# Kernel optimization log

Measured on AMD Instinct MI355X. Metric: run time of the kernel, lower is better.

## Reference

```python
import jax, jax.numpy as jnp
import numpy as np

B, F, S, H1, H2 = 4096, 512, 32, 64, 32


def setup_inputs() -> dict:
    key = jax.random.key(0)
    ks = jax.random.split(key, 9)
    x = jax.random.normal(ks[0], (B, F), dtype=jnp.float32)
    # ExU layer init: truncated_normal(mean=4, std=0.5) on weight, std=0.5 on bias
    W0 = 4.0 + 0.5 * jax.random.normal(ks[1], (F, S, S), dtype=jnp.float32)
    b0 = 0.5 * jax.random.normal(ks[2], (F, S), dtype=jnp.float32)
    # ReLU hidden layers: xavier-ish weights, small biases
    W1 = jax.random.normal(ks[3], (F, S, H1), dtype=jnp.float32) * np.sqrt(2.0 / (S + H1))
    b1 = 0.5 * jax.random.normal(ks[4], (F, S), dtype=jnp.float32)
    W2 = jax.random.normal(ks[5], (F, H1, H2), dtype=jnp.float32) * np.sqrt(2.0 / (H1 + H2))
    b2 = 0.5 * jax.random.normal(ks[6], (F, H1), dtype=jnp.float32)
    Wl = jax.random.normal(ks[7], (F, H2), dtype=jnp.float32) * np.sqrt(2.0 / (H2 + 1))
    out_bias = jnp.zeros((1,), dtype=jnp.float32)
    return {"x": x, "W0": W0, "b0": b0, "W1": W1, "b1": b1,
            "W2": W2, "b2": b2, "Wl": Wl, "out_bias": out_bias}


def reference(x, W0, b0, W1, b1, W2, b2, Wl, out_bias):
    # ExU shallow layer per feature: clip((x_f - b0_f) @ exp(W0_f), 0, 1)
    # x[:, :, None] - b0 broadcasts scalar feature to (B, F, S)
    h = jnp.clip(jnp.einsum('bfs,fsh->bfh', x[:, :, None] - b0[None], jnp.exp(W0)), 0.0, 1.0)
    # ReLU hidden layers: relu((h - b) @ W)
    h = jax.nn.relu(jnp.einsum('bfs,fsh->bfh', h - b1[None], W1))   # (B, F, H1)
    h = jax.nn.relu(jnp.einsum('bfh,fho->bfo', h - b2[None], W2))   # (B, F, H2)
    # per-feature Linear(H2 -> 1, no bias), concatenated over features
    f_out = jnp.einsum('bfo,fo->bf', h, Wl)                          # (B, F)
    # forward_type == 'sum' (feature_dropout is identity at inference)
    return f_out.sum(axis=-1) + out_bias[0], f_out
```

## Files before the change

kernel.cpp:

```cpp
#include <hip/hip_runtime.h>

typedef __attribute__((ext_vector_type(8))) short short8;
typedef __attribute__((ext_vector_type(4))) float f32x4;
typedef unsigned int uint32;

namespace {
constexpr int F = 512, NB = 4096;
constexpr int RB = 1024;
constexpr int FPB = 4;
constexpr int NFQ = F / FPB;
constexpr size_t OFF_W1F  = 0;
constexpr size_t OFF_W2F  = OFF_W1F + (size_t)F * 4 * 64 * 16;
constexpr size_t OFF_TAB  = OFF_W2F + (size_t)F * 4 * 64 * 16;
constexpr size_t OFF_PART = OFF_TAB + (size_t)F * 160 * 4;
constexpr size_t WS_NEED  = OFF_PART + (size_t)NFQ * NB * 4;
}

__device__ __forceinline__ uint32 cvtpk(float lo, float hi) {
    uint32 r;
    asm("v_cvt_pk_bf16_f32 %0, %1, %2" : "=v"(r) : "v"(lo), "v"(hi));
    return r;
}
__device__ __forceinline__ float clip01(float v) {
    return __builtin_amdgcn_fmed3f(v, 0.f, 1.f);
}

__global__ __launch_bounds__(256) void nam_prep(
    const float* __restrict__ W0, const float* __restrict__ b0,
    const float* __restrict__ W1, const float* __restrict__ b1,
    const float* __restrict__ W2, const float* __restrict__ b2,
    char* __restrict__ ws)
{
    const int f = blockIdx.x;
    const int t = threadIdx.x;
    const int lane = t & 63, w = t >> 6, g = lane >> 4, rr = lane & 15;

    __shared__ float LW[2048];
    __shared__ float red[256], red2[256];

    const float* W0f = W0 + (size_t)f * 1024;
    const float* W1f = W1 + (size_t)f * 2048;
    const float* W2f = W2 + (size_t)f * 2048;
    float* tab = (float*)(ws + OFF_TAB) + (size_t)f * 160;
    union U8 { uint32 u[4]; short8 s8; };

    *(float4*)&LW[t * 4] = *(const float4*)&W0f[t * 4];
    __syncthreads();
    {
        int j = t & 31, sc = t >> 5;
        float a = 0.f, c = 0.f;
#pragma unroll
        for (int k = 0; k < 4; ++k) {
            int s = sc * 4 + k;
            float e = expf(LW[s * 32 + j]);
            a += e; c += b0[f * 32 + s] * e;
        }
        red[sc * 32 + j] = a; red2[sc * 32 + j] = c;
    }
    __syncthreads();
    if (t < 32) {
        float a = 0.f, c = 0.f;
#pragma unroll
        for (int k = 0; k < 8; ++k) { a += red[k * 32 + t]; c += red2[k * 32 + t]; }
        tab[t] = a; tab[32 + t] = -c;
    }
    __syncthreads();

    *(float4*)&LW[t * 4]        = *(const float4*)&W1f[t * 4];
    *(float4*)&LW[1024 + t * 4] = *(const float4*)&W1f[1024 + t * 4];
    __syncthreads();
    {
        int j = t & 63, sc = t >> 6;
        float d = 0.f;
#pragma unroll
        for (int k = 0; k < 8; ++k) {
            int s = sc * 8 + k;
            d += b1[f * 32 + s] * LW[s * 64 + j];
        }
        red[sc * 64 + j] = d;
    }
    {
        int mi = w;
        int col = 32 * (mi & 1) + 8 * (rr >> 2) + 4 * (mi >> 1) + (rr & 3);
        int base = (8 * g) * 64 + col;
        U8 v;
        v.u[0] = cvtpk(LW[base],       LW[base + 64]);
        v.u[1] = cvtpk(LW[base + 128], LW[base + 192]);
        v.u[2] = cvtpk(LW[base + 256], LW[base + 320]);
        v.u[3] = cvtpk(LW[base + 384], LW[base + 448]);
        ((short8*)(ws + OFF_W1F))[((size_t)f * 4 + mi) * 64 + lane] = v.s8;
    }
    __syncthreads();
    if (t < 64) {
        float d = red[t] + red[64 + t] + red[128 + t] + red[192 + t];
        int dst = 32 * ((t >> 2) & 1) + 16 * (t >> 5) + 4 * ((t >> 3) & 3) + (t & 3);
        tab[64 + dst] = -d;
    }
    __syncthreads();

    *(float4*)&LW[t * 4]        = *(const float4*)&W2f[t * 4];
    *(float4*)&LW[1024 + t * 4] = *(const float4*)&W2f[1024 + t * 4];
    __syncthreads();
    {
        int o = t & 31, hc = t >> 5;
        float d = 0.f;
#pragma unroll
        for (int k = 0; k < 8; ++k) {
            int h = hc * 8 + k;
            d += b2[f * 64 + h] * LW[h * 32 + o];
        }
        red[hc * 32 + o] = d;
    }
    {
        int m2 = w >> 1, kc = w & 1;
        int base = (32 * kc + 8 * g) * 32 + 16 * m2 + rr;
        U8 v;
        v.u[0] = cvtpk(LW[base],       LW[base + 32]);
        v.u[1] = cvtpk(LW[base + 64],  LW[base + 96]);
        v.u[2] = cvtpk(LW[base + 128], LW[base + 160]);
        v.u[3] = cvtpk(LW[base + 192], LW[base + 224]);
        ((short8*)(ws + OFF_W2F))[((size_t)f * 4 + m2 * 2 + kc) * 64 + lane] = v.s8;
    }
    __syncthreads();
    if (t < 32) {
        float d = 0.f;
#pragma unroll
        for (int k = 0; k < 8; ++k) d += red[k * 32 + t];
        tab[128 + t] = -d;
    }
}

__device__ __forceinline__ void tile_compute(
    float xv, const short8* w1f, const short8 (&w2f)[2][2],
    const f32x4& A0, const f32x4& A1, const f32x4& C0, const f32x4& C1,
    const f32x4* nd1, const f32x4* nd2, f32x4& c0, f32x4& c1)
{
    union U8 { uint32 u[4]; short8 s8; };
    U8 hb;
    hb.u[0] = cvtpk(clip01(fmaf(xv, A0[0], C0[0])), clip01(fmaf(xv, A0[1], C0[1])));
    hb.u[1] = cvtpk(clip01(fmaf(xv, A0[2], C0[2])), clip01(fmaf(xv, A0[3], C0[3])));
    hb.u[2] = cvtpk(clip01(fmaf(xv, A1[0], C1[0])), clip01(fmaf(xv, A1[1], C1[1])));
    hb.u[3] = cvtpk(clip01(fmaf(xv, A1[2], C1[2])), clip01(fmaf(xv, A1[3], C1[3])));
    short8 b0f = hb.s8;

    f32x4 a0 = __builtin_amdgcn_mfma_f32_16x16x32_bf16(w1f[0], b0f, nd1[0], 0, 0, 0);
    f32x4 a1 = __builtin_amdgcn_mfma_f32_16x16x32_bf16(w1f[1], b0f, nd1[1], 0, 0, 0);
    f32x4 a2 = __builtin_amdgcn_mfma_f32_16x16x32_bf16(w1f[2], b0f, nd1[2], 0, 0, 0);
    f32x4 a3 = __builtin_amdgcn_mfma_f32_16x16x32_bf16(w1f[3], b0f, nd1[3], 0, 0, 0);

    U8 r0, r1;
    r0.u[0] = cvtpk(fmaxf(a0[0], 0.f), fmaxf(a0[1], 0.f));
    r0.u[1] = cvtpk(fmaxf(a0[2], 0.f), fmaxf(a0[3], 0.f));
    r0.u[2] = cvtpk(fmaxf(a2[0], 0.f), fmaxf(a2[1], 0.f));
    r0.u[3] = cvtpk(fmaxf(a2[2], 0.f), fmaxf(a2[3], 0.f));
    r1.u[0] = cvtpk(fmaxf(a1[0], 0.f), fmaxf(a1[1], 0.f));
    r1.u[1] = cvtpk(fmaxf(a1[2], 0.f), fmaxf(a1[3], 0.f));
    r1.u[2] = cvtpk(fmaxf(a3[0], 0.f), fmaxf(a3[1], 0.f));
    r1.u[3] = cvtpk(fmaxf(a3[2], 0.f), fmaxf(a3[3], 0.f));

    c0 = __builtin_amdgcn_mfma_f32_16x16x32_bf16(w2f[0][0], r0.s8, nd2[0], 0, 0, 0);
    c0 = __builtin_amdgcn_mfma_f32_16x16x32_bf16(w2f[0][1], r1.s8, c0, 0, 0, 0);
    c1 = __builtin_amdgcn_mfma_f32_16x16x32_bf16(w2f[1][0], r0.s8, nd2[1], 0, 0, 0);
    c1 = __builtin_amdgcn_mfma_f32_16x16x32_bf16(w2f[1][1], r1.s8, c1, 0, 0, 0);
}

__global__ __launch_bounds__(256, 2) void nam_main(
    const float* __restrict__ x, const float* __restrict__ Wl,
    const char* __restrict__ ws, float* __restrict__ fout, float* __restrict__ part)
{
    const int fq = blockIdx.y;
    const int f0 = fq * FPB;
    const int rbase = blockIdx.x * RB;
    const int t = threadIdx.x;
    const int w = t >> 6, lane = t & 63;
    const int g = lane >> 4, rr = lane & 15;
    const int f = f0 + w;

    __shared__ float sx[FPB * RB];
    __shared__ float sfo[FPB * RB];

#pragma unroll
    for (int kk = 0; kk < 4; ++kk) {
        int r = t + 256 * kk;
        float4 v = *(const float4*)(x + (size_t)(rbase + r) * F + f0);
        sx[0 * RB + r] = v.x; sx[1 * RB + r] = v.y;
        sx[2 * RB + r] = v.z; sx[3 * RB + r] = v.w;
    }

    const short8* w1img = (const short8*)(ws + OFF_W1F);
    const short8* w2img = (const short8*)(ws + OFF_W2F);
    short8 w1f[4], w2f[2][2];
#pragma unroll
    for (int mi = 0; mi < 4; ++mi) w1f[mi] = w1img[((size_t)f * 4 + mi) * 64 + lane];
#pragma unroll
    for (int m2 = 0; m2 < 2; ++m2)
#pragma unroll
        for (int kc = 0; kc < 2; ++kc)
            w2f[m2][kc] = w2img[((size_t)f * 4 + m2 * 2 + kc) * 64 + lane];

    const f32x4* tabv = (const f32x4*)((const float*)(ws + OFF_TAB) + (size_t)f * 160);
    f32x4 A0 = tabv[2 * g], A1 = tabv[2 * g + 1];
    f32x4 C0 = tabv[8 + 2 * g], C1 = tabv[8 + 2 * g + 1];
    f32x4 nd1[4];
#pragma unroll
    for (int mi = 0; mi < 4; ++mi) nd1[mi] = tabv[16 + 4 * mi + g];
    f32x4 nd2[2];
#pragma unroll
    for (int m2 = 0; m2 < 2; ++m2) nd2[m2] = tabv[32 + 4 * m2 + g];
    f32x4 wl0 = *(const f32x4*)(Wl + f * 32 + 4 * g);
    f32x4 wl1 = *(const f32x4*)(Wl + f * 32 + 16 + 4 * g);

    __syncthreads();

    const float* sxf = sx + w * RB;
    float* sfof = sfo + w * RB;

    for (int k = 0; k < 32; ++k) {
        float xv0 = sxf[32 * k + rr];
        float xv1 = sxf[32 * k + 16 + rr];
        f32x4 c00, c01, c10, c11;
        tile_compute(xv0, w1f, w2f, A0, A1, C0, C1, nd1, nd2, c00, c01);
        tile_compute(xv1, w1f, w2f, A0, A1, C0, C1, nd1, nd2, c10, c11);

        float p0 = 0.f, p1 = 0.f;
#pragma unroll
        for (int r = 0; r < 4; ++r) {
            p0 = fmaf(fmaxf(c00[r], 0.f), wl0[r], p0);
            p0 = fmaf(fmaxf(c01[r], 0.f), wl1[r], p0);
            p1 = fmaf(fmaxf(c10[r], 0.f), wl0[r], p1);
            p1 = fmaf(fmaxf(c11[r], 0.f), wl1[r], p1);
        }
        p0 += __shfl_xor(p0, 16, 64);
        p0 += __shfl_xor(p0, 32, 64);
        p1 += __shfl_xor(p1, 16, 64);
        p1 += __shfl_xor(p1, 32, 64);
        if (lane < 16) {
            sfof[32 * k + lane] = p0;
            sfof[32 * k + 16 + lane] = p1;
        }
    }

    __syncthreads();

#pragma unroll
    for (int kk = 0; kk < 4; ++kk) {
        int r = t + 256 * kk;
        float v0 = sfo[0 * RB + r], v1 = sfo[1 * RB + r];
        float v2 = sfo[2 * RB + r], v3 = sfo[3 * RB + r];
        *(float4*)(fout + (size_t)(rbase + r) * F + f0) = make_float4(v0, v1, v2, v3);
        part[(size_t)fq * NB + rbase + r] = (v0 + v1) + (v2 + v3);
    }
}

__global__ __launch_bounds__(256) void nam_sum(const float* __restrict__ part,
                                               const float* __restrict__ ob,
                                               float* __restrict__ out0) {
    int r = blockIdx.x * 256 + threadIdx.x;
    float s = ob[0];
#pragma unroll 8
    for (int q = 0; q < NFQ; ++q) s += part[(size_t)q * NB + r];
    out0[r] = s;
}

namespace fbk { constexpr int S = 32, H1 = 64, H2 = 32, BLK = 256, ROWS = 2, P1 = 36; }
__global__ __launch_bounds__(256, 2) void fb_main(
    const float* __restrict__ x,  const float* __restrict__ W0,
    const float* __restrict__ b0, const float* __restrict__ W1,
    const float* __restrict__ b1, const float* __restrict__ W2,
    const float* __restrict__ b2, const float* __restrict__ Wl,
    float* __restrict__ fout) {
    using namespace fbk;
    const int f = blockIdx.y;
    const int bbase = blockIdx.x * (BLK * ROWS);
    const int t = threadIdx.x;
    __shared__ float W0e[S * S];
    __shared__ float W1t[H1 * P1];
    __shared__ float W2l[H1 * H2];
    __shared__ float sb0[S], sb1[S], sb2[H1];
    __shared__ float sA[S], sC[S], sd1[H1], sd2[H2], sWl[H2];
    {
        float4 wv = *reinterpret_cast<const float4*>(W0 + (size_t)f * S * S + t * 4);
        W0e[t * 4 + 0] = expf(wv.x); W0e[t * 4 + 1] = expf(wv.y);
        W0e[t * 4 + 2] = expf(wv.z); W0e[t * 4 + 3] = expf(wv.w);
    }
    if (t < S) sb0[t] = b0[f * S + t];
    else if (t < 2 * S) sb1[t - S] = b1[f * S + (t - S)];
    else if (t < 2 * S + H1) sb2[t - 2 * S] = b2[f * H1 + (t - 2 * S)];
    else if (t < 2 * S + H1 + H2) sWl[t - 2 * S - H1] = Wl[f * H2 + (t - 2 * S - H1)];
#pragma unroll
    for (int k = 0; k < (S * H1) / BLK; ++k) {
        int i = t + BLK * k; int s = i >> 6, j = i & 63;
        W1t[j * P1 + s] = W1[(size_t)f * S * H1 + i];
    }
#pragma unroll
    for (int k = 0; k < (H1 * H2) / BLK; ++k) {
        int i = t + BLK * k; W2l[i] = W2[(size_t)f * H1 * H2 + i];
    }
    __syncthreads();
    if (t < S) {
        int j = t; float a = 0.f, c = 0.f;
#pragma unroll
        for (int s = 0; s < S; ++s) { float e = W0e[s * S + j]; a += e; c += sb0[s] * e; }
        sA[j] = a; sC[j] = c;
    } else if (t >= 64 && t < 64 + H1) {
        int j = t - 64; float d = 0.f;
#pragma unroll
        for (int s = 0; s < S; ++s) d += sb1[s] * W1t[j * P1 + s];
        sd1[j] = d;
    } else if (t >= 128 && t < 128 + H2) {
        int o = t - 128; float d = 0.f;
#pragma unroll
        for (int h = 0; h < H1; ++h) d += sb2[h] * W2l[h * H2 + o];
        sd2[o] = d;
    }
    __syncthreads();
    const int ra = bbase + t, rb = bbase + BLK + t;
    const float xa = x[(size_t)ra * F + f], xb = x[(size_t)rb * F + f];
    float h0a[S], h0b[S];
#pragma unroll
    for (int j = 0; j < S; ++j) {
        float A = sA[j], C = sC[j];
        h0a[j] = fminf(fmaxf(fmaf(xa, A, -C), 0.f), 1.f);
        h0b[j] = fminf(fmaxf(fmaf(xb, A, -C), 0.f), 1.f);
    }
    float acc2a[H2], acc2b[H2];
#pragma unroll
    for (int o = 0; o < H2; ++o) { float d = sd2[o]; acc2a[o] = -d; acc2b[o] = -d; }
#pragma unroll 2
    for (int j = 0; j < H1; ++j) {
        float wr[S];
#pragma unroll
        for (int q = 0; q < S / 4; ++q)
            *reinterpret_cast<float4*>(&wr[4 * q]) = reinterpret_cast<const float4*>(&W1t[j * P1])[q];
        float d1j = sd1[j];
        float pa0 = -d1j, pa1 = 0.f, pb0 = -d1j, pb1 = 0.f;
#pragma unroll
        for (int s = 0; s < S; s += 2) {
            pa0 = fmaf(h0a[s], wr[s], pa0); pb0 = fmaf(h0b[s], wr[s], pb0);
            pa1 = fmaf(h0a[s + 1], wr[s + 1], pa1); pb1 = fmaf(h0b[s + 1], wr[s + 1], pb1);
        }
        float h1a = fmaxf(pa0 + pa1, 0.f), h1b = fmaxf(pb0 + pb1, 0.f);
        float w2r[H2];
#pragma unroll
        for (int q = 0; q < H2 / 4; ++q)
            *reinterpret_cast<float4*>(&w2r[4 * q]) = reinterpret_cast<const float4*>(&W2l[j * H2])[q];
#pragma unroll
        for (int o = 0; o < H2; ++o) {
            acc2a[o] = fmaf(h1a, w2r[o], acc2a[o]); acc2b[o] = fmaf(h1b, w2r[o], acc2b[o]);
        }
    }
    float outa = 0.f, outb = 0.f;
#pragma unroll
    for (int o = 0; o < H2; ++o) {
        outa = fmaf(fmaxf(acc2a[o], 0.f), sWl[o], outa);
        outb = fmaf(fmaxf(acc2b[o], 0.f), sWl[o], outb);
    }
    fout[(size_t)ra * F + f] = outa;
    fout[(size_t)rb * F + f] = outb;
}
__global__ __launch_bounds__(256) void fb_rowsum(
    const float* __restrict__ fout, const float* __restrict__ out_bias,
    float* __restrict__ out0) {
    const int wave = threadIdx.x >> 6, lane = threadIdx.x & 63;
    const int b = blockIdx.x * 4 + wave;
    float s = 0.f;
#pragma unroll
    for (int k = 0; k < F / 64; ++k) s += fout[(size_t)b * F + k * 64 + lane];
#pragma unroll
    for (int off = 32; off; off >>= 1) s += __shfl_down(s, off, 64);
    if (lane == 0) out0[b] = s + out_bias[0];
}

extern "C" void kernel_launch(void* const* d_in, const int* in_sizes, int n_in,
                              void* d_out, int out_size, void* d_ws, size_t ws_size,
                              hipStream_t stream) {
    const float* x  = (const float*)d_in[0];
    const float* W0 = (const float*)d_in[1];
    const float* b0 = (const float*)d_in[2];
    const float* W1 = (const float*)d_in[3];
    const float* b1 = (const float*)d_in[4];
    const float* W2 = (const float*)d_in[5];
    const float* b2 = (const float*)d_in[6];
    const float* Wl = (const float*)d_in[7];
    const float* ob = (const float*)d_in[8];

    float* out0 = (float*)d_out;
    float* fout = out0 + NB;

    if (ws_size >= WS_NEED) {
        char* ws = (char*)d_ws;
        float* part = (float*)(ws + OFF_PART);
        nam_prep<<<F, 256, 0, stream>>>(W0, b0, W1, b1, W2, b2, ws);
        nam_main<<<dim3(NB / RB, NFQ), 256, 0, stream>>>(x, Wl, ws, fout, part);
        nam_sum <<<NB / 256, 256, 0, stream>>>(part, ob, out0);
    } else {
        dim3 grid(NB / (fbk::BLK * fbk::ROWS), F);
        fb_main<<<grid, fbk::BLK, 0, stream>>>(x, W0, b0, W1, b1, W2, b2, Wl, fout);
        fb_rowsum<<<NB / 4, 256, 0, stream>>>(fout, ob, out0);
    }
}
```

Measured before the change: 54.03 us.

## Interleave MFMA chains via inline asm and halve per-block row tile

Replaces the compiler-scheduled MFMA builtins with inline-asm MFMA instructions grouped so that the two row tiles' independent MFMAs issue back to back. Manual sched_barriers and s_nop padding handle the VALU/MFMA hazards. The row block size drops from 1024 to 512, which doubles the grid and halves LDS use per block. The intent is better MFMA pipeline utilisation and occupancy. The risk is that the hand-inserted nops are wasted or insufficient, and that smaller blocks reload weights more often.

```diff
diff --git a/kernel.cpp b/kernel.cpp
--- a/kernel.cpp
+++ b/kernel.cpp
@@ -6,7 +6,7 @@
 
 namespace {
 constexpr int F = 512, NB = 4096;
-constexpr int RB = 1024;
+constexpr int RB = 512;
 constexpr int FPB = 4;
 constexpr int NFQ = F / FPB;
 constexpr size_t OFF_W1F  = 0;
@@ -24,6 +24,20 @@
 __device__ __forceinline__ float clip01(float v) {
     return __builtin_amdgcn_fmed3f(v, 0.f, 1.f);
 }
+
+__device__ __forceinline__ f32x4 mfma_init(short8 a, short8 b, f32x4 c) {
+    f32x4 d;
+    asm("v_mfma_f32_16x16x32_bf16 %0, %1, %2, %3"
+        : "=&v"(d) : "v"(a), "v"(b), "v"(c));
+    return d;
+}
+__device__ __forceinline__ void mfma_acc(f32x4& c, short8 a, short8 b) {
+    asm("v_mfma_f32_16x16x32_bf16 %0, %1, %2, %0"
+        : "+v"(c) : "v"(a), "v"(b));
+}
+#define SBAR()      __builtin_amdgcn_sched_barrier(0)
+#define NOP_VM()    asm volatile("s_nop 1")
+#define NOP_MV()    asm volatile("s_nop 7\n\ts_nop 7")
 
 __global__ __launch_bounds__(256) void nam_prep(
     const float* __restrict__ W0, const float* __restrict__ b0,
@@ -130,38 +144,22 @@
     }
 }
 
-__device__ __forceinline__ void tile_compute(
-    float xv, const short8* w1f, const short8 (&w2f)[2][2],
-    const f32x4& A0, const f32x4& A1, const f32x4& C0, const f32x4& C1,
-    const f32x4* nd1, const f32x4* nd2, f32x4& c0, f32x4& c1)
-{
-    union U8 { uint32 u[4]; short8 s8; };
-    U8 hb;
+__device__ __forceinline__ short8 make_hb(float xv, const f32x4& A0, const f32x4& A1,
+                                          const f32x4& C0, const f32x4& C1) {
+    union { uint32 u[4]; short8 s8; } hb;
     hb.u[0] = cvtpk(clip01(fmaf(xv, A0[0], C0[0])), clip01(fmaf(xv, A0[1], C0[1])));
     hb.u[1] = cvtpk(clip01(fmaf(xv, A0[2], C0[2])), clip01(fmaf(xv, A0[3], C0[3])));
     hb.u[2] = cvtpk(clip01(fmaf(xv, A1[0], C1[0])), clip01(fmaf(xv, A1[1], C1[1])));
     hb.u[3] = cvtpk(clip01(fmaf(xv, A1[2], C1[2])), clip01(fmaf(xv, A1[3], C1[3])));
-    short8 b0f = hb.s8;
-
-    f32x4 a0 = __builtin_amdgcn_mfma_f32_16x16x32_bf16(w1f[0], b0f, nd1[0], 0, 0, 0);
-    f32x4 a1 = __builtin_amdgcn_mfma_f32_16x16x32_bf16(w1f[1], b0f, nd1[1], 0, 0, 0);
-    f32x4 a2 = __builtin_amdgcn_mfma_f32_16x16x32_bf16(w1f[2], b0f, nd1[2], 0, 0, 0);
-    f32x4 a3 = __builtin_amdgcn_mfma_f32_16x16x32_bf16(w1f[3], b0f, nd1[3], 0, 0, 0);
-
-    U8 r0, r1;
-    r0.u[0] = cvtpk(fmaxf(a0[0], 0.f), fmaxf(a0[1], 0.f));
-    r0.u[1] = cvtpk(fmaxf(a0[2], 0.f), fmaxf(a0[3], 0.f));
-    r0.u[2] = cvtpk(fmaxf(a2[0], 0.f), fmaxf(a2[1], 0.f));
-    r0.u[3] = cvtpk(fmaxf(a2[2], 0.f), fmaxf(a2[3], 0.f));
-    r1.u[0] = cvtpk(fmaxf(a1[0], 0.f), fmaxf(a1[1], 0.f));
-    r1.u[1] = cvtpk(fmaxf(a1[2], 0.f), fmaxf(a1[3], 0.f));
-    r1.u[2] = cvtpk(fmaxf(a3[0], 0.f), fmaxf(a3[1], 0.f));
-    r1.u[3] = cvtpk(fmaxf(a3[2], 0.f), fmaxf(a3[3], 0.f));
-
-    c0 = __builtin_amdgcn_mfma_f32_16x16x32_bf16(w2f[0][0], r0.s8, nd2[0], 0, 0, 0);
-    c0 = __builtin_amdgcn_mfma_f32_16x16x32_bf16(w2f[0][1], r1.s8, c0, 0, 0, 0);
-    c1 = __builtin_amdgcn_mfma_f32_16x16x32_bf16(w2f[1][0], r0.s8, nd2[1], 0, 0, 0);
-    c1 = __builtin_amdgcn_mfma_f32_16x16x32_bf16(w2f[1][1], r1.s8, c1, 0, 0, 0);
+    return hb.s8;
+}
+__device__ __forceinline__ short8 packrelu(const f32x4& x, const f32x4& y) {
+    union { uint32 u[4]; short8 s8; } r;
+    r.u[0] = cvtpk(fmaxf(x[0], 0.f), fmaxf(x[1], 0.f));
+    r.u[1] = cvtpk(fmaxf(x[2], 0.f), fmaxf(x[3], 0.f));
+    r.u[2] = cvtpk(fmaxf(y[0], 0.f), fmaxf(y[1], 0.f));
+    r.u[3] = cvtpk(fmaxf(y[2], 0.f), fmaxf(y[3], 0.f));
+    return r.s8;
 }
 
 __global__ __launch_bounds__(256, 2) void nam_main(
@@ -180,7 +178,7 @@
     __shared__ float sfo[FPB * RB];
 
 #pragma unroll
-    for (int kk = 0; kk < 4; ++kk) {
+    for (int kk = 0; kk < 2; ++kk) {
         int r = t + 256 * kk;
         float4 v = *(const float4*)(x + (size_t)(rbase + r) * F + f0);
         sx[0 * RB + r] = v.x; sx[1 * RB + r] = v.y;
@@ -215,12 +213,39 @@
     const float* sxf = sx + w * RB;
     float* sfof = sfo + w * RB;
 
-    for (int k = 0; k < 32; ++k) {
+    for (int k = 0; k < 16; ++k) {
         float xv0 = sxf[32 * k + rr];
         float xv1 = sxf[32 * k + 16 + rr];
-        f32x4 c00, c01, c10, c11;
-        tile_compute(xv0, w1f, w2f, A0, A1, C0, C1, nd1, nd2, c00, c01);
-        tile_compute(xv1, w1f, w2f, A0, A1, C0, C1, nd1, nd2, c10, c11);
+
+        short8 hb0 = make_hb(xv0, A0, A1, C0, C1);
+        short8 hb1 = make_hb(xv1, A0, A1, C0, C1);
+
+        SBAR(); NOP_VM();
+        f32x4 a00 = mfma_init(w1f[0], hb0, nd1[0]);
+        f32x4 a01 = mfma_init(w1f[1], hb0, nd1[1]);
+        f32x4 a02 = mfma_init(w1f[2], hb0, nd1[2]);
+        f32x4 a03 = mfma_init(w1f[3], hb0, nd1[3]);
+        f32x4 a10 = mfma_init(w1f[0], hb1, nd1[0]);
+        f32x4 a11 = mfma_init(w1f[1], hb1, nd1[1]);
+        f32x4 a12 = mfma_init(w1f[2], hb1, nd1[2]);
+        f32x4 a13 = mfma_init(w1f[3], hb1, nd1[3]);
+        SBAR(); NOP_MV();
+
+        short8 r00 = packrelu(a00, a02);
+        short8 r01 = packrelu(a01, a03);
+        short8 r10 = packrelu(a10, a12);
+        short8 r11 = packrelu(a11, a13);
+
+        SBAR(); NOP_VM();
+        f32x4 c00 = mfma_init(w2f[0][0], r00, nd2[0]);
+        f32x4 c01 = mfma_init(w2f[1][0], r00, nd2[1]);
+        f32x4 c10 = mfma_init(w2f[0][0], r10, nd2[0]);
+        f32x4 c11 = mfma_init(w2f[1][0], r10, nd2[1]);
+        mfma_acc(c00, w2f[0][1], r01);
+        mfma_acc(c01, w2f[1][1], r01);
+        mfma_acc(c10, w2f[0][1], r11);
+        mfma_acc(c11, w2f[1][1], r11);
+        SBAR(); NOP_MV();
 
         float p0 = 0.f, p1 = 0.f;
 #pragma unroll
@@ -243,7 +268,7 @@
     __syncthreads();
 
 #pragma unroll
-    for (int kk = 0; kk < 4; ++kk) {
+    for (int kk = 0; kk < 2; ++kk) {
         int r = t + 256 * kk;
         float v0 = sfo[0 * RB + r], v1 = sfo[1 * RB + r];
         float v2 = sfo[2 * RB + r], v3 = sfo[3 * RB + r];
```

Result: faster. 48.95 us (-9.4%).
